# Optimization experiments

Hardware: AMD Instinct MI355X
Metric: run time of the kernel (lower is better)

## Reference

```python
import jax, jax.numpy as jnp
import numpy as np

N, E, D, H, C = 100000, 1600000, 128, 128, 47
EPS = 1e-5


def setup_inputs() -> dict:
    key = jax.random.key(0)
    ks = jax.random.split(key, 10)
    s = 1.0 / np.sqrt(D).astype(np.float32)
    return {
        "x": jax.random.normal(ks[0], (N, D), jnp.float32),
        "edge_index": jax.random.randint(ks[1], (2, E), 0, N, jnp.int32),
        "Wl0": jax.random.normal(ks[2], (H, D), jnp.float32) * s,
        "bl0": jnp.zeros((H,), jnp.float32),
        "Wr0": jax.random.normal(ks[3], (H, D), jnp.float32) * s,
        "g0": jnp.ones((H,), jnp.float32),
        "b0": jnp.zeros((H,), jnp.float32),
        "Wl1": jax.random.normal(ks[4], (H, H), jnp.float32) * s,
        "bl1": jnp.zeros((H,), jnp.float32),
        "Wr1": jax.random.normal(ks[5], (H, H), jnp.float32) * s,
        "g1": jnp.ones((H,), jnp.float32),
        "b1": jnp.zeros((H,), jnp.float32),
        "Wl2": jax.random.normal(ks[6], (C, H), jnp.float32) * s,
        "bl2": jnp.zeros((C,), jnp.float32),
        "Wr2": jax.random.normal(ks[7], (C, H), jnp.float32) * s,
    }


def _sage_conv(x, edge_index, Wl, bl, Wr):
    # PyG SAGEConv(mean aggr): out = lin_l(mean_{j in N(i)} x_j) + lin_r(x_i)
    dst, src = edge_index[0], edge_index[1]
    n = x.shape[0]
    msg = x[src]                                             # [E, d] gather
    summed = jax.ops.segment_sum(msg, dst, num_segments=n)   # [N, d] scatter-add
    deg = jax.ops.segment_sum(jnp.ones((msg.shape[0],), x.dtype), dst, num_segments=n)
    agg = summed / jnp.maximum(deg, 1.0)[:, None]            # mean over neighbors
    return agg @ Wl.T + bl + x @ Wr.T


def _bn(x, g, b):
    # BatchNorm1d, training-mode batch statistics (biased variance)
    mu = jnp.mean(x, axis=0)
    var = jnp.mean(jnp.square(x - mu), axis=0)
    return (x - mu) * jax.lax.rsqrt(var + EPS) * g + b


def reference(x, edge_index, Wl0, bl0, Wr0, g0, b0, Wl1, bl1, Wr1, g1, b1, Wl2, bl2, Wr2):
    h = _sage_conv(x, edge_index, Wl0, bl0, Wr0)
    h = jax.nn.relu(_bn(h, g0, b0))          # dropout treated as identity (deterministic reference)
    h = _sage_conv(h, edge_index, Wl1, bl1, Wr1)
    h = jax.nn.relu(_bn(h, g1, b1))
    return _sage_conv(h, edge_index, Wl2, bl2, Wr2)
```

## Files before the change

kernel.cpp:

```cpp
#include <hip/hip_runtime.h>

typedef __attribute__((ext_vector_type(8))) short short8;
typedef __attribute__((ext_vector_type(4))) float f32x4;

constexpr float BN_EPS = 1e-5f;
#define NBUCKETS 128
#define SLOT 24576

__device__ __forceinline__ ushort f2bf(float f) {
  uint u = __float_as_uint(f);
  u = (u + 0x7fffu + ((u >> 16) & 1u)) >> 16;
  return (ushort)u;
}
__device__ __forceinline__ float bf2f(ushort h) { return __uint_as_float((uint)h << 16); }
__device__ __forceinline__ float bf2f_lo(uint v) { return __uint_as_float(v << 16); }
__device__ __forceinline__ float bf2f_hi(uint v) { return __uint_as_float(v & 0xffff0000u); }

typedef __attribute__((address_space(1))) const unsigned int* as1_cu32;
typedef __attribute__((address_space(3))) unsigned int* as3_u32;
__device__ __forceinline__ void gload_lds16(const void* g, void* l) {
  __builtin_amdgcn_global_load_lds((as1_cu32)g, (as3_u32)l, 16, 0, 0);
}


__global__ __launch_bounds__(256) void k_cast(const float* __restrict__ in, ushort* __restrict__ out, int n4) {
  for (int i = blockIdx.x * 256 + threadIdx.x; i < n4; i += gridDim.x * 256) {
    float4 v = reinterpret_cast<const float4*>(in)[i];
    ushort4 o;
    o.x = f2bf(v.x); o.y = f2bf(v.y); o.z = f2bf(v.z); o.w = f2bf(v.w);
    reinterpret_cast<ushort4*>(out)[i] = o;
  }
}

__global__ __launch_bounds__(256) void k_prep_init(const float* __restrict__ Wl0, const float* __restrict__ Wr0,
                                                   const float* __restrict__ Wl1, const float* __restrict__ Wr1,
                                                   const float* __restrict__ Wl2, const float* __restrict__ Wr2,
                                                   ushort* __restrict__ W0l, ushort* __restrict__ W0r,
                                                   ushort* __restrict__ W1l, ushort* __restrict__ W1r,
                                                   ushort* __restrict__ Wc, int* __restrict__ bcur,
                                                   float* __restrict__ statsAll, int C) {
  int b = blockIdx.x;
  if (b < 64) {
    const float* src = (b < 16) ? Wl0 : (b < 32) ? Wr0 : (b < 48) ? Wl1 : Wr1;
    ushort* dst = (b < 16) ? W0l : (b < 32) ? W0r : (b < 48) ? W1l : W1r;
    int i = (b & 15) * 256 + threadIdx.x;
    float4 v = reinterpret_cast<const float4*>(src)[i];
    ushort4 o;
    o.x = f2bf(v.x); o.y = f2bf(v.y); o.z = f2bf(v.z); o.w = f2bf(v.w);
    reinterpret_cast<ushort4*>(dst)[i] = o;
  } else if (b < 128) {
    int i = (b - 64) * 256 + threadIdx.x;
    int r = i >> 7, k = i & 127;
    float v = 0.f;
    if (r < C) v = Wl2[r * 128 + k];
    else if (r >= 64 && r < 64 + C) v = Wr2[(r - 64) * 128 + k];
    Wc[i] = f2bf(v);
  } else {
    if (threadIdx.x < NBUCKETS) bcur[threadIdx.x] = threadIdx.x * SLOT;
    for (int i = threadIdx.x; i < 512; i += 256) statsAll[i] = 0.f;
  }
}


__global__ __launch_bounds__(256) void k_binscatter(const int* __restrict__ dst, const int* __restrict__ src, int E,
                                                    int* __restrict__ bcur, uint* __restrict__ ebuf) {
  __shared__ int h[NBUCKETS];
  __shared__ int base[NBUCKETS];
  __shared__ int cur[NBUCKETS];
  const int e0 = blockIdx.x * 8192;
  const int e1 = min(e0 + 8192, E);
  for (int i = threadIdx.x; i < NBUCKETS; i += 256) h[i] = 0;
  __syncthreads();
  for (int e = e0 + threadIdx.x * 4; e < e1; e += 1024) {
    int4 d = *reinterpret_cast<const int4*>(&dst[e]);
    if (e + 3 < e1) {
      atomicAdd(&h[d.x >> 10], 1); atomicAdd(&h[d.y >> 10], 1);
      atomicAdd(&h[d.z >> 10], 1); atomicAdd(&h[d.w >> 10], 1);
    } else {
      for (int j = 0; e + j < e1; ++j) atomicAdd(&h[dst[e + j] >> 10], 1);
    }
  }
  __syncthreads();
  if (threadIdx.x < NBUCKETS) {
    base[threadIdx.x] = atomicAdd(&bcur[threadIdx.x], h[threadIdx.x]);
    cur[threadIdx.x] = 0;
  }
  __syncthreads();
  for (int e = e0 + threadIdx.x * 4; e < e1; e += 1024) {
    int4 d = *reinterpret_cast<const int4*>(&dst[e]);
    int4 s = *reinterpret_cast<const int4*>(&src[e]);
    int dd[4] = {d.x, d.y, d.z, d.w};
    int ss[4] = {s.x, s.y, s.z, s.w};
    for (int j = 0; j < 4 && e + j < e1; ++j) {
      int b = dd[j] >> 10;
      int pos = base[b] + atomicAdd(&cur[b], 1);
      ebuf[pos] = (uint)(dd[j] & 1023) | ((uint)ss[j] << 10);
    }
  }
}

__global__ __launch_bounds__(512) void k_bucket_build(const uint* __restrict__ ebuf, const int* __restrict__ bend,
                                                      int* __restrict__ rp, int* __restrict__ deg,
                                                      float* __restrict__ deg_inv, int* __restrict__ csr, int N) {
  __shared__ int cnt[1024];
  __shared__ int pre[1024];
  __shared__ int tmp[1024];
  const int blk = blockIdx.x, tid = threadIdx.x;
  const int base = blk << 10;
  const int p0 = blk * SLOT, p1 = bend[blk];
  for (int i = tid; i < 1024; i += 512) cnt[i] = 0;
  __syncthreads();
  for (int p = p0 + tid; p < p1; p += 512) atomicAdd(&cnt[ebuf[p] & 1023u], 1);
  __syncthreads();
  for (int i = tid; i < 1024; i += 512) pre[i] = cnt[i];
  __syncthreads();
  for (int off = 1; off < 1024; off <<= 1) {
    for (int i = tid; i < 1024; i += 512) tmp[i] = (i >= off) ? pre[i - off] : 0;
    __syncthreads();
    for (int i = tid; i < 1024; i += 512) pre[i] += tmp[i];
    __syncthreads();
  }
  for (int i = tid; i < 1024; i += 512) {
    int node = base + i;
    if (node < N) {
      int c = cnt[i];
      rp[node] = p0 + pre[i] - c;
      deg[node] = c;
      deg_inv[node] = 1.0f / (float)max(c, 1);
    }
    tmp[i] = pre[i] - cnt[i];
  }
  __syncthreads();
  for (int p = p0 + tid; p < p1; p += 512) {
    uint pr = ebuf[p];
    int pos = p0 + atomicAdd(&tmp[pr & 1023u], 1);
    csr[pos] = (int)(pr >> 10);
  }
}


__global__ __launch_bounds__(512, 4) void k_fused(const ushort* __restrict__ X, const ushort* __restrict__ Bsrc,
                                                  const ushort* __restrict__ WA, const ushort* __restrict__ WB,
                                                  const int* __restrict__ rp, const int* __restrict__ deg,
                                                  const float* __restrict__ deg_inv, const int* __restrict__ csr,
                                                  float* __restrict__ partial, ushort* __restrict__ Z, int M) {
  __shared__ ushort sA[64 * 128];
  __shared__ ushort sB[64 * 128];
  const int tid = threadIdx.x;
  const int wave = tid >> 6, lane = tid & 63;
  const int rfrag = lane & 15, kgrp = lane >> 4;
  const int li = rfrag;
  const int row0 = blockIdx.x * 64;

#pragma unroll
  for (int i = 0; i < 2; ++i) {
    int c = wave * 2 + i;
    int lb = c * 1024 + lane * 16;
    int row = lb >> 8, bin = lb & 255;
    int gr = min(row0 + row, M - 1);
    int sb = bin ^ ((row & 7) << 4);
    gload_lds16((const char*)Bsrc + (size_t)gr * 256 + sb, (char*)sB + c * 1024);
  }

  const uint4* X16 = reinterpret_cast<const uint4*>(X);
#pragma unroll
  for (int g = 0; g < 2; ++g) {
    const int lrow = wave * 8 + g * 4 + kgrp;
    const int node = row0 + lrow;
    float a0 = 0.f, a1 = 0.f, a2 = 0.f, a3 = 0.f, a4 = 0.f, a5 = 0.f, a6 = 0.f, a7 = 0.f;
    if (node < M) {
      const int start = rp[node];
      const int c = deg[node];
      int p = 0;
      for (; p + 7 < c; p += 8) {
        int idx[8];
#pragma unroll
        for (int u = 0; u < 8; ++u) idx[u] = csr[start + p + u];
        uint4 v[8];
#pragma unroll
        for (int u = 0; u < 8; ++u) v[u] = X16[(size_t)idx[u] * 16 + li];
#pragma unroll
        for (int u = 0; u < 8; ++u) {
          a0 += bf2f_lo(v[u].x); a1 += bf2f_hi(v[u].x);
          a2 += bf2f_lo(v[u].y); a3 += bf2f_hi(v[u].y);
          a4 += bf2f_lo(v[u].z); a5 += bf2f_hi(v[u].z);
          a6 += bf2f_lo(v[u].w); a7 += bf2f_hi(v[u].w);
        }
      }
      if (p + 3 < c) {
        int idx[4];
#pragma unroll
        for (int u = 0; u < 4; ++u) idx[u] = csr[start + p + u];
        uint4 v[4];
#pragma unroll
        for (int u = 0; u < 4; ++u) v[u] = X16[(size_t)idx[u] * 16 + li];
#pragma unroll
        for (int u = 0; u < 4; ++u) {
          a0 += bf2f_lo(v[u].x); a1 += bf2f_hi(v[u].x);
          a2 += bf2f_lo(v[u].y); a3 += bf2f_hi(v[u].y);
          a4 += bf2f_lo(v[u].z); a5 += bf2f_hi(v[u].z);
          a6 += bf2f_lo(v[u].w); a7 += bf2f_hi(v[u].w);
        }
        p += 4;
      }
      for (; p < c; ++p) {
        uint4 v = X16[(size_t)csr[start + p] * 16 + li];
        a0 += bf2f_lo(v.x); a1 += bf2f_hi(v.x);
        a2 += bf2f_lo(v.y); a3 += bf2f_hi(v.y);
        a4 += bf2f_lo(v.z); a5 += bf2f_hi(v.z);
        a6 += bf2f_lo(v.w); a7 += bf2f_hi(v.w);
      }
      const float di = deg_inv[node];
      a0 *= di; a1 *= di; a2 *= di; a3 *= di;
      a4 *= di; a5 *= di; a6 *= di; a7 *= di;
    }
    uint4 o;
    o.x = (uint)f2bf(a0) | ((uint)f2bf(a1) << 16);
    o.y = (uint)f2bf(a2) | ((uint)f2bf(a3) << 16);
    o.z = (uint)f2bf(a4) | ((uint)f2bf(a5) << 16);
    o.w = (uint)f2bf(a6) | ((uint)f2bf(a7) << 16);
    *reinterpret_cast<uint4*>((char*)sA + lrow * 256 + ((li * 16) ^ ((lrow & 7) << 4))) = o;
  }

  short8 wfA[4], wfB[4];
  {
    const ushort* wa = WA + (wave * 16 + rfrag) * 128 + kgrp * 8;
    const ushort* wb = WB + (wave * 16 + rfrag) * 128 + kgrp * 8;
#pragma unroll
    for (int s = 0; s < 4; ++s) {
      wfA[s] = *reinterpret_cast<const short8*>(wa + s * 32);
      wfB[s] = *reinterpret_cast<const short8*>(wb + s * 32);
    }
  }
  __syncthreads();

  f32x4 acc[4];
#pragma unroll
  for (int i = 0; i < 4; ++i) acc[i] = (f32x4){0.f, 0.f, 0.f, 0.f};

  const int rs = (rfrag & 7) << 4;
#pragma unroll
  for (int strip = 0; strip < 4; ++strip) {
    const int r = strip * 16 + rfrag;
    short8 af[4], bf[4];
#pragma unroll
    for (int s = 0; s < 4; ++s) {
      int off = (kgrp * 16 + s * 64) ^ rs;
      af[s] = *reinterpret_cast<const short8*>((const char*)sA + r * 256 + off);
      bf[s] = *reinterpret_cast<const short8*>((const char*)sB + r * 256 + off);
    }
#pragma unroll
    for (int s = 0; s < 4; ++s)
      acc[strip] = __builtin_amdgcn_mfma_f32_16x16x32_bf16(af[s], wfA[s], acc[strip], 0, 0, 0);
#pragma unroll
    for (int s = 0; s < 4; ++s)
      acc[strip] = __builtin_amdgcn_mfma_f32_16x16x32_bf16(bf[s], wfB[s], acc[strip], 0, 0, 0);
  }

  {
    float s1 = 0.f, s2 = 0.f;
#pragma unroll
    for (int strip = 0; strip < 4; ++strip) {
#pragma unroll
      for (int rr = 0; rr < 4; ++rr) {
        int grow = row0 + strip * 16 + kgrp * 4 + rr;
        if (grow < M) {
          float v = acc[strip][rr];
          s1 += v;
          s2 = fmaf(v, v, s2);
        }
      }
    }
    s1 += __shfl_xor(s1, 16); s2 += __shfl_xor(s2, 16);
    s1 += __shfl_xor(s1, 32); s2 += __shfl_xor(s2, 32);
    if (kgrp == 0) {
      partial[(size_t)blockIdx.x * 256 + wave * 16 + rfrag] = s1;
      partial[(size_t)blockIdx.x * 256 + 128 + wave * 16 + rfrag] = s2;
    }
  }
  __syncthreads();

  const int cb = (wave * 16 + rfrag) * 2;
#pragma unroll
  for (int strip = 0; strip < 4; ++strip) {
#pragma unroll
    for (int rr = 0; rr < 4; ++rr) {
      int row = strip * 16 + kgrp * 4 + rr;
      *reinterpret_cast<ushort*>((char*)sA + row * 256 + (cb ^ ((row & 7) << 4))) = f2bf(acc[strip][rr]);
    }
  }
  __syncthreads();

#pragma unroll
  for (int i = 0; i < 2; ++i) {
    int lb = (wave * 2 + i) * 1024 + lane * 16;
    int row = lb >> 8, bin = lb & 255;
    int gr = row0 + row;
    if (gr < M)
      *reinterpret_cast<uint4*>((char*)Z + (size_t)gr * 256 + bin) =
          *reinterpret_cast<const uint4*>((const char*)sA + row * 256 + (bin ^ ((row & 7) << 4)));
  }
}


__global__ __launch_bounds__(512, 6) void k_gemm1(const ushort* __restrict__ H, const ushort* __restrict__ Wc,
                                                  ushort* __restrict__ Yb, ushort* __restrict__ Rb, int M) {
  __shared__ ushort sA[64 * 128];
  const int tid = threadIdx.x;
  const int wave = tid >> 6, lane = tid & 63;
  const int rfrag = lane & 15, kgrp = lane >> 4;
  const int row0 = blockIdx.x * 64;

#pragma unroll
  for (int i = 0; i < 2; ++i) {
    int c = wave * 2 + i;
    int lb = c * 1024 + lane * 16;
    int row = lb >> 8, bin = lb & 255;
    int gr = min(row0 + row, M - 1);
    int sb = bin ^ ((row & 7) << 4);
    gload_lds16((const char*)H + (size_t)gr * 256 + sb, (char*)sA + c * 1024);
  }

  short8 wf[4];
  {
    const ushort* wp = Wc + (wave * 16 + rfrag) * 128 + kgrp * 8;
#pragma unroll
    for (int s = 0; s < 4; ++s) wf[s] = *reinterpret_cast<const short8*>(wp + s * 32);
  }
  __syncthreads();

  f32x4 acc[4];
#pragma unroll
  for (int i = 0; i < 4; ++i) acc[i] = (f32x4){0.f, 0.f, 0.f, 0.f};
  const int rs = (rfrag & 7) << 4;
#pragma unroll
  for (int strip = 0; strip < 4; ++strip) {
    const int r = strip * 16 + rfrag;
    short8 af[4];
#pragma unroll
    for (int s = 0; s < 4; ++s)
      af[s] = *reinterpret_cast<const short8*>((const char*)sA + r * 256 + ((kgrp * 16 + s * 64) ^ rs));
#pragma unroll
    for (int s = 0; s < 4; ++s)
      acc[strip] = __builtin_amdgcn_mfma_f32_16x16x32_bf16(af[s], wf[s], acc[strip], 0, 0, 0);
  }
  __syncthreads();

  const int cb = (wave * 16 + rfrag) * 2;
#pragma unroll
  for (int strip = 0; strip < 4; ++strip) {
#pragma unroll
    for (int rr = 0; rr < 4; ++rr) {
      int row = strip * 16 + kgrp * 4 + rr;
      *reinterpret_cast<ushort*>((char*)sA + row * 256 + (cb ^ ((row & 7) << 4))) = f2bf(acc[strip][rr]);
    }
  }
  __syncthreads();

#pragma unroll
  for (int i = 0; i < 2; ++i) {
    int lb = (wave * 2 + i) * 1024 + lane * 16;
    int row = lb >> 8, bin = lb & 255;
    int gr = row0 + row;
    if (gr < M) {
      uint4 v = *reinterpret_cast<const uint4*>((const char*)sA + row * 256 + (bin ^ ((row & 7) << 4)));
      if (bin < 128) *reinterpret_cast<uint4*>((char*)Yb + (size_t)gr * 128 + bin) = v;
      else *reinterpret_cast<uint4*>((char*)Rb + (size_t)gr * 128 + (bin - 128)) = v;
    }
  }
}


__global__ __launch_bounds__(256) void k_bn_reduce(const float* __restrict__ partial, int nblk,
                                                   float* __restrict__ stats) {
  float acc = 0.f;
  for (int b = blockIdx.x; b < nblk; b += gridDim.x) acc += partial[(size_t)b * 256 + threadIdx.x];
  atomicAdd(&stats[threadIdx.x], acc);
}

__global__ __launch_bounds__(256) void k_bn_relu(uint2* __restrict__ Z, int n2, const float* __restrict__ sums,
                                                 const float* __restrict__ g, const float* __restrict__ b,
                                                 float invM) {
  __shared__ float ss[256];
  if (threadIdx.x < 128) {
    int f = threadIdx.x;
    float mean = sums[f] * invM;
    float var = fmaxf(sums[128 + f] * invM - mean * mean, 0.f);
    float sc = g[f] * rsqrtf(var + BN_EPS);
    ss[f] = sc;
    ss[128 + f] = fmaf(-mean, sc, b[f]);
  }
  __syncthreads();
  for (int i = blockIdx.x * 256 + threadIdx.x; i < n2; i += gridDim.x * 256) {
    uint2 v = Z[i];
    int f0 = (i & 31) * 4;
    float a0 = fmaxf(fmaf(bf2f_lo(v.x), ss[f0 + 0], ss[128 + f0 + 0]), 0.f);
    float a1 = fmaxf(fmaf(bf2f_hi(v.x), ss[f0 + 1], ss[128 + f0 + 1]), 0.f);
    float a2 = fmaxf(fmaf(bf2f_lo(v.y), ss[f0 + 2], ss[128 + f0 + 2]), 0.f);
    float a3 = fmaxf(fmaf(bf2f_hi(v.y), ss[f0 + 3], ss[128 + f0 + 3]), 0.f);
    v.x = (uint)f2bf(a0) | ((uint)f2bf(a1) << 16);
    v.y = (uint)f2bf(a2) | ((uint)f2bf(a3) << 16);
    Z[i] = v;
  }
}


__global__ __launch_bounds__(256) void k_agg47(const ushort* __restrict__ Yb, const ushort* __restrict__ Rb,
                                               const float* __restrict__ bias, const int* __restrict__ rp,
                                               const int* __restrict__ deg, const float* __restrict__ deg_inv,
                                               const int* __restrict__ csr, float* __restrict__ out,
                                               int N, int C) {
  const int wave = threadIdx.x >> 6, lane = threadIdx.x & 63;
  const int sub = lane >> 3, li = lane & 7;
  const int node = blockIdx.x * 32 + wave * 8 + sub;
  if (node >= N) return;
  const int start = rp[node];
  const int c = deg[node];
  const uint4* Y16 = reinterpret_cast<const uint4*>(Yb);
  float a0 = 0.f, a1 = 0.f, a2 = 0.f, a3 = 0.f, a4 = 0.f, a5 = 0.f, a6 = 0.f, a7 = 0.f;
  int p = 0;
  for (; p + 7 < c; p += 8) {
    int idx[8];
#pragma unroll
    for (int u = 0; u < 8; ++u) idx[u] = csr[start + p + u];
    uint4 v[8];
#pragma unroll
    for (int u = 0; u < 8; ++u) v[u] = Y16[(size_t)idx[u] * 8 + li];
#pragma unroll
    for (int u = 0; u < 8; ++u) {
      a0 += bf2f_lo(v[u].x); a1 += bf2f_hi(v[u].x);
      a2 += bf2f_lo(v[u].y); a3 += bf2f_hi(v[u].y);
      a4 += bf2f_lo(v[u].z); a5 += bf2f_hi(v[u].z);
      a6 += bf2f_lo(v[u].w); a7 += bf2f_hi(v[u].w);
    }
  }
  for (; p < c; ++p) {
    uint4 v = Y16[(size_t)csr[start + p] * 8 + li];
    a0 += bf2f_lo(v.x); a1 += bf2f_hi(v.x);
    a2 += bf2f_lo(v.y); a3 += bf2f_hi(v.y);
    a4 += bf2f_lo(v.z); a5 += bf2f_hi(v.z);
    a6 += bf2f_lo(v.w); a7 += bf2f_hi(v.w);
  }
  const float di = deg_inv[node];
  uint4 sv = reinterpret_cast<const uint4*>(Rb)[(size_t)node * 8 + li];
  float s[8] = {bf2f_lo(sv.x), bf2f_hi(sv.x), bf2f_lo(sv.y), bf2f_hi(sv.y),
                bf2f_lo(sv.z), bf2f_hi(sv.z), bf2f_lo(sv.w), bf2f_hi(sv.w)};
  float a[8] = {a0, a1, a2, a3, a4, a5, a6, a7};
#pragma unroll
  for (int j = 0; j < 8; ++j) {
    int f = li * 8 + j;
    if (f < C) out[(size_t)node * C + f] = fmaf(a[j], di, s[j] + bias[f]);
  }
}


extern "C" void kernel_launch(void* const* d_in, const int* in_sizes, int n_in,
                              void* d_out, int out_size, void* d_ws, size_t ws_size,
                              hipStream_t stream) {
  const float* x   = (const float*)d_in[0];
  const int*   ei  = (const int*)d_in[1];
  const float* Wl0 = (const float*)d_in[2];
  const float* Wr0 = (const float*)d_in[4];
  const float* g0  = (const float*)d_in[5];
  const float* b0  = (const float*)d_in[6];
  const float* Wl1 = (const float*)d_in[7];
  const float* Wr1 = (const float*)d_in[9];
  const float* g1  = (const float*)d_in[10];
  const float* b1  = (const float*)d_in[11];
  const float* Wl2 = (const float*)d_in[12];
  const float* bl2 = (const float*)d_in[13];
  const float* Wr2 = (const float*)d_in[14];

  const int N = in_sizes[0] / 128;
  const int E = in_sizes[1] / 2;
  const int C = in_sizes[13];

  const int* edst = ei;
  const int* esrc = ei + E;

  char* w = (char*)d_ws;
  auto al = [](size_t v) { return (v + 255) & ~(size_t)255; };
  size_t off = 0;
  int*    bcur    = (int*)(w + off);    off = al(off + NBUCKETS * 4);
  float*  stats   = (float*)(w + off);  off = al(off + 512 * 4);
  int*    rp      = (int*)(w + off);    off = al(off + (size_t)N * 4);
  int*    deg     = (int*)(w + off);    off = al(off + (size_t)N * 4);
  float*  deg_inv = (float*)(w + off);  off = al(off + (size_t)N * 4);
  int*    csr     = (int*)(w + off);    off = al(off + (size_t)NBUCKETS * SLOT * 4);
  uint*   ebuf    = (uint*)(w + off);   off = al(off + (size_t)NBUCKETS * SLOT * 4);
  ushort* Xb      = (ushort*)(w + off); off = al(off + (size_t)N * 128 * 2);
  ushort* hA      = (ushort*)(w + off); off = al(off + (size_t)N * 128 * 2);
  ushort* hB      = (ushort*)(w + off); off = al(off + (size_t)N * 128 * 2);
  ushort* W0l     = (ushort*)(w + off); off = al(off + 16384 * 2);
  ushort* W0r     = (ushort*)(w + off); off = al(off + 16384 * 2);
  ushort* W1l     = (ushort*)(w + off); off = al(off + 16384 * 2);
  ushort* W1r     = (ushort*)(w + off); off = al(off + 16384 * 2);
  ushort* Wc      = (ushort*)(w + off); off = al(off + 16384 * 2);
  const int nblkG = (N + 63) / 64;
  float*  partial = (float*)(w + off);  off = al(off + (size_t)nblkG * 256 * 4);

  float* stats0 = stats;
  float* stats1 = stats + 256;
  ushort* Yb = hB;
  ushort* Rb = hB + (size_t)N * 64;

  const int binGrid = (E + 8191) / 8192;
  const int nbBuck = (N + 1023) / 1024;
  const int agg47Grid = (N + 31) / 32;
  const float invM = 1.0f / (float)N;

  k_cast<<<2048, 256, 0, stream>>>(x, Xb, N * 32);
  k_prep_init<<<129, 256, 0, stream>>>(Wl0, Wr0, Wl1, Wr1, Wl2, Wr2, W0l, W0r, W1l, W1r, Wc,
                                       bcur, stats, C);

  k_binscatter<<<binGrid, 256, 0, stream>>>(edst, esrc, E, bcur, ebuf);
  k_bucket_build<<<nbBuck, 512, 0, stream>>>(ebuf, bcur, rp, deg, deg_inv, csr, N);

  k_fused<<<nblkG, 512, 0, stream>>>(Xb, Xb, W0l, W0r, rp, deg, deg_inv, csr, partial, hB, N);
  k_bn_reduce<<<64, 256, 0, stream>>>(partial, nblkG, stats0);
  k_bn_relu<<<2048, 256, 0, stream>>>((uint2*)hB, N * 32, stats0, g0, b0, invM);

  k_fused<<<nblkG, 512, 0, stream>>>(hB, hB, W1l, W1r, rp, deg, deg_inv, csr, partial, hA, N);
  k_bn_reduce<<<64, 256, 0, stream>>>(partial, nblkG, stats1);
  k_bn_relu<<<2048, 256, 0, stream>>>((uint2*)hA, N * 32, stats1, g1, b1, invM);

  k_gemm1<<<nblkG, 512, 0, stream>>>(hA, Wc, Yb, Rb, N);
  k_agg47<<<agg47Grid, 256, 0, stream>>>(Yb, Rb, bl2, rp, deg, deg_inv, csr, (float*)d_out, N, C);
}
```

Measured before the change: 314.1 us.

## Fuse BN+ReLU into consumer kernels and merge prep kernels into one launch

Removes the separate BN-reduce and BN-ReLU passes. Per-block statistics are now accumulated with global atomics, and the normalize+ReLU step is applied on the fly by the next kernel: inside the neighbor gather, on the self-row tile in LDS, and in the final GEMM. The cast, weight-prep and edge bin-scatter kernels are merged into one launch, with bucket cursors reset by a memset. In exchange, every gathered neighbor row now pays extra FMAs, and float atomics make the statistics order-dependent.

```diff
diff --git a/kernel.cpp b/kernel.cpp
--- a/kernel.cpp
+++ b/kernel.cpp
@@ -23,80 +23,85 @@
 }
 
 
-__global__ __launch_bounds__(256) void k_cast(const float* __restrict__ in, ushort* __restrict__ out, int n4) {
-  for (int i = blockIdx.x * 256 + threadIdx.x; i < n4; i += gridDim.x * 256) {
-    float4 v = reinterpret_cast<const float4*>(in)[i];
+__global__ __launch_bounds__(256) void k_prep(const int* __restrict__ dst, const int* __restrict__ src, int E,
+                                              int* __restrict__ bcur, uint* __restrict__ ebuf,
+                                              const float* __restrict__ x, ushort* __restrict__ Xb, int n4,
+                                              const float* __restrict__ Wl0, const float* __restrict__ Wr0,
+                                              const float* __restrict__ Wl1, const float* __restrict__ Wr1,
+                                              const float* __restrict__ Wl2, const float* __restrict__ Wr2,
+                                              ushort* __restrict__ W0l, ushort* __restrict__ W0r,
+                                              ushort* __restrict__ W1l, ushort* __restrict__ W1r,
+                                              ushort* __restrict__ Wc, float* __restrict__ statsAll,
+                                              int C, int binGrid, int castGrid) {
+  int bb = blockIdx.x;
+  if (bb < binGrid) {
+    __shared__ int h[NBUCKETS];
+    __shared__ int base[NBUCKETS];
+    __shared__ int cur[NBUCKETS];
+    const int e0 = bb * 8192;
+    const int e1 = min(e0 + 8192, E);
+    for (int i = threadIdx.x; i < NBUCKETS; i += 256) h[i] = 0;
+    __syncthreads();
+    for (int e = e0 + threadIdx.x * 4; e < e1; e += 1024) {
+      int4 d = *reinterpret_cast<const int4*>(&dst[e]);
+      if (e + 3 < e1) {
+        atomicAdd(&h[d.x >> 10], 1); atomicAdd(&h[d.y >> 10], 1);
+        atomicAdd(&h[d.z >> 10], 1); atomicAdd(&h[d.w >> 10], 1);
+      } else {
+        for (int j = 0; e + j < e1; ++j) atomicAdd(&h[dst[e + j] >> 10], 1);
+      }
+    }
+    __syncthreads();
+    if (threadIdx.x < NBUCKETS) {
+      base[threadIdx.x] = threadIdx.x * SLOT + atomicAdd(&bcur[threadIdx.x], h[threadIdx.x]);
+      cur[threadIdx.x] = 0;
+    }
+    __syncthreads();
+    for (int e = e0 + threadIdx.x * 4; e < e1; e += 1024) {
+      int4 d = *reinterpret_cast<const int4*>(&dst[e]);
+      int4 s = *reinterpret_cast<const int4*>(&src[e]);
+      int dd[4] = {d.x, d.y, d.z, d.w};
+      int ss[4] = {s.x, s.y, s.z, s.w};
+      for (int j = 0; j < 4 && e + j < e1; ++j) {
+        int b = dd[j] >> 10;
+        int pos = base[b] + atomicAdd(&cur[b], 1);
+        ebuf[pos] = (uint)(dd[j] & 1023) | ((uint)ss[j] << 10);
+      }
+    }
+    return;
+  }
+  bb -= binGrid;
+  if (bb < 64) {
+    const float* s = (bb < 16) ? Wl0 : (bb < 32) ? Wr0 : (bb < 48) ? Wl1 : Wr1;
+    ushort* d = (bb < 16) ? W0l : (bb < 32) ? W0r : (bb < 48) ? W1l : W1r;
+    int i = (bb & 15) * 256 + threadIdx.x;
+    float4 v = reinterpret_cast<const float4*>(s)[i];
     ushort4 o;
     o.x = f2bf(v.x); o.y = f2bf(v.y); o.z = f2bf(v.z); o.w = f2bf(v.w);
-    reinterpret_cast<ushort4*>(out)[i] = o;
-  }
-}
-
-__global__ __launch_bounds__(256) void k_prep_init(const float* __restrict__ Wl0, const float* __restrict__ Wr0,
-                                                   const float* __restrict__ Wl1, const float* __restrict__ Wr1,
-                                                   const float* __restrict__ Wl2, const float* __restrict__ Wr2,
-                                                   ushort* __restrict__ W0l, ushort* __restrict__ W0r,
-                                                   ushort* __restrict__ W1l, ushort* __restrict__ W1r,
-                                                   ushort* __restrict__ Wc, int* __restrict__ bcur,
-                                                   float* __restrict__ statsAll, int C) {
-  int b = blockIdx.x;
-  if (b < 64) {
-    const float* src = (b < 16) ? Wl0 : (b < 32) ? Wr0 : (b < 48) ? Wl1 : Wr1;
-    ushort* dst = (b < 16) ? W0l : (b < 32) ? W0r : (b < 48) ? W1l : W1r;
-    int i = (b & 15) * 256 + threadIdx.x;
-    float4 v = reinterpret_cast<const float4*>(src)[i];
-    ushort4 o;
-    o.x = f2bf(v.x); o.y = f2bf(v.y); o.z = f2bf(v.z); o.w = f2bf(v.w);
-    reinterpret_cast<ushort4*>(dst)[i] = o;
-  } else if (b < 128) {
-    int i = (b - 64) * 256 + threadIdx.x;
+    reinterpret_cast<ushort4*>(d)[i] = o;
+    return;
+  }
+  bb -= 64;
+  if (bb < 64) {
+    int i = bb * 256 + threadIdx.x;
     int r = i >> 7, k = i & 127;
     float v = 0.f;
     if (r < C) v = Wl2[r * 128 + k];
     else if (r >= 64 && r < 64 + C) v = Wr2[(r - 64) * 128 + k];
     Wc[i] = f2bf(v);
-  } else {
-    if (threadIdx.x < NBUCKETS) bcur[threadIdx.x] = threadIdx.x * SLOT;
-    for (int i = threadIdx.x; i < 512; i += 256) statsAll[i] = 0.f;
-  }
-}
-
-
-__global__ __launch_bounds__(256) void k_binscatter(const int* __restrict__ dst, const int* __restrict__ src, int E,
-                                                    int* __restrict__ bcur, uint* __restrict__ ebuf) {
-  __shared__ int h[NBUCKETS];
-  __shared__ int base[NBUCKETS];
-  __shared__ int cur[NBUCKETS];
-  const int e0 = blockIdx.x * 8192;
-  const int e1 = min(e0 + 8192, E);
-  for (int i = threadIdx.x; i < NBUCKETS; i += 256) h[i] = 0;
-  __syncthreads();
-  for (int e = e0 + threadIdx.x * 4; e < e1; e += 1024) {
-    int4 d = *reinterpret_cast<const int4*>(&dst[e]);
-    if (e + 3 < e1) {
-      atomicAdd(&h[d.x >> 10], 1); atomicAdd(&h[d.y >> 10], 1);
-      atomicAdd(&h[d.z >> 10], 1); atomicAdd(&h[d.w >> 10], 1);
-    } else {
-      for (int j = 0; e + j < e1; ++j) atomicAdd(&h[dst[e + j] >> 10], 1);
-    }
-  }
-  __syncthreads();
-  if (threadIdx.x < NBUCKETS) {
-    base[threadIdx.x] = atomicAdd(&bcur[threadIdx.x], h[threadIdx.x]);
-    cur[threadIdx.x] = 0;
-  }
-  __syncthreads();
-  for (int e = e0 + threadIdx.x * 4; e < e1; e += 1024) {
-    int4 d = *reinterpret_cast<const int4*>(&dst[e]);
-    int4 s = *reinterpret_cast<const int4*>(&src[e]);
-    int dd[4] = {d.x, d.y, d.z, d.w};
-    int ss[4] = {s.x, s.y, s.z, s.w};
-    for (int j = 0; j < 4 && e + j < e1; ++j) {
-      int b = dd[j] >> 10;
-      int pos = base[b] + atomicAdd(&cur[b], 1);
-      ebuf[pos] = (uint)(dd[j] & 1023) | ((uint)ss[j] << 10);
-    }
-  }
+    return;
+  }
+  bb -= 64;
+  if (bb < castGrid) {
+    for (int i = bb * 256 + threadIdx.x; i < n4; i += castGrid * 256) {
+      float4 v = reinterpret_cast<const float4*>(x)[i];
+      ushort4 o;
+      o.x = f2bf(v.x); o.y = f2bf(v.y); o.z = f2bf(v.z); o.w = f2bf(v.w);
+      reinterpret_cast<ushort4*>(Xb)[i] = o;
+    }
+    return;
+  }
+  for (int i = threadIdx.x; i < 512; i += 256) statsAll[i] = 0.f;
 }
 
 __global__ __launch_bounds__(512) void k_bucket_build(const uint* __restrict__ ebuf, const int* __restrict__ bend,
@@ -107,7 +112,7 @@
   __shared__ int tmp[1024];
   const int blk = blockIdx.x, tid = threadIdx.x;
   const int base = blk << 10;
-  const int p0 = blk * SLOT, p1 = bend[blk];
+  const int p0 = blk * SLOT, p1 = p0 + bend[blk];
   for (int i = tid; i < 1024; i += 512) cnt[i] = 0;
   __syncthreads();
   for (int p = p0 + tid; p < p1; p += 512) atomicAdd(&cnt[ebuf[p] & 1023u], 1);
@@ -139,18 +144,31 @@
 }
 
 
+template <bool PRE_BN>
 __global__ __launch_bounds__(512, 4) void k_fused(const ushort* __restrict__ X, const ushort* __restrict__ Bsrc,
                                                   const ushort* __restrict__ WA, const ushort* __restrict__ WB,
                                                   const int* __restrict__ rp, const int* __restrict__ deg,
                                                   const float* __restrict__ deg_inv, const int* __restrict__ csr,
-                                                  float* __restrict__ partial, ushort* __restrict__ Z, int M) {
+                                                  const float* __restrict__ sums, const float* __restrict__ gw,
+                                                  const float* __restrict__ bw, float invM,
+                                                  float* __restrict__ stats_out, ushort* __restrict__ Z, int M) {
   __shared__ ushort sA[64 * 128];
   __shared__ ushort sB[64 * 128];
+  __shared__ float ssc[PRE_BN ? 128 : 1];
+  __shared__ float ssh[PRE_BN ? 128 : 1];
   const int tid = threadIdx.x;
   const int wave = tid >> 6, lane = tid & 63;
   const int rfrag = lane & 15, kgrp = lane >> 4;
   const int li = rfrag;
   const int row0 = blockIdx.x * 64;
+
+  if (PRE_BN && tid < 128) {
+    float mean = sums[tid] * invM;
+    float var = fmaxf(sums[128 + tid] * invM - mean * mean, 0.f);
+    float sc = gw[tid] * rsqrtf(var + BN_EPS);
+    ssc[tid] = sc;
+    ssh[tid] = fmaf(-mean, sc, bw[tid]);
+  }
 
 #pragma unroll
   for (int i = 0; i < 2; ++i) {
@@ -160,6 +178,28 @@
     int gr = min(row0 + row, M - 1);
     int sb = bin ^ ((row & 7) << 4);
     gload_lds16((const char*)Bsrc + (size_t)gr * 256 + sb, (char*)sB + c * 1024);
+  }
+
+  float scr[8], shr[8];
+  if (PRE_BN) {
+#pragma unroll
+    for (int e = 0; e < 8; ++e) {
+      int f = li * 8 + e;
+      float mean = sums[f] * invM;
+      float var = fmaxf(sums[128 + f] * invM - mean * mean, 0.f);
+      scr[e] = gw[f] * rsqrtf(var + BN_EPS);
+      shr[e] = fmaf(-mean, scr[e], bw[f]);
+    }
+  }
+
+#define BN8(vv, A0, A1, e0)                                                     \
+  {                                                                             \
+    float xl = bf2f_lo(vv), xh = bf2f_hi(vv);                                   \
+    if (PRE_BN) {                                                               \
+      xl = fmaxf(fmaf(xl, scr[e0], shr[e0]), 0.f);                              \
+      xh = fmaxf(fmaf(xh, scr[e0 + 1], shr[e0 + 1]), 0.f);                      \
+    }                                                                           \
+    A0 += xl; A1 += xh;                                                         \
   }
 
   const uint4* X16 = reinterpret_cast<const uint4*>(X);
@@ -181,10 +221,8 @@
         for (int u = 0; u < 8; ++u) v[u] = X16[(size_t)idx[u] * 16 + li];
 #pragma unroll
         for (int u = 0; u < 8; ++u) {
-          a0 += bf2f_lo(v[u].x); a1 += bf2f_hi(v[u].x);
-          a2 += bf2f_lo(v[u].y); a3 += bf2f_hi(v[u].y);
-          a4 += bf2f_lo(v[u].z); a5 += bf2f_hi(v[u].z);
-          a6 += bf2f_lo(v[u].w); a7 += bf2f_hi(v[u].w);
+          BN8(v[u].x, a0, a1, 0); BN8(v[u].y, a2, a3, 2);
+          BN8(v[u].z, a4, a5, 4); BN8(v[u].w, a6, a7, 6);
         }
       }
       if (p + 3 < c) {
@@ -196,19 +234,15 @@
         for (int u = 0; u < 4; ++u) v[u] = X16[(size_t)idx[u] * 16 + li];
 #pragma unroll
         for (int u = 0; u < 4; ++u) {
-          a0 += bf2f_lo(v[u].x); a1 += bf2f_hi(v[u].x);
-          a2 += bf2f_lo(v[u].y); a3 += bf2f_hi(v[u].y);
-          a4 += bf2f_lo(v[u].z); a5 += bf2f_hi(v[u].z);
-          a6 += bf2f_lo(v[u].w); a7 += bf2f_hi(v[u].w);
+          BN8(v[u].x, a0, a1, 0); BN8(v[u].y, a2, a3, 2);
+          BN8(v[u].z, a4, a5, 4); BN8(v[u].w, a6, a7, 6);
         }
         p += 4;
       }
       for (; p < c; ++p) {
         uint4 v = X16[(size_t)csr[start + p] * 16 + li];
-        a0 += bf2f_lo(v.x); a1 += bf2f_hi(v.x);
-        a2 += bf2f_lo(v.y); a3 += bf2f_hi(v.y);
-        a4 += bf2f_lo(v.z); a5 += bf2f_hi(v.z);
-        a6 += bf2f_lo(v.w); a7 += bf2f_hi(v.w);
+        BN8(v.x, a0, a1, 0); BN8(v.y, a2, a3, 2);
+        BN8(v.z, a4, a5, 4); BN8(v.w, a6, a7, 6);
       }
       const float di = deg_inv[node];
       a0 *= di; a1 *= di; a2 *= di; a3 *= di;
@@ -221,6 +255,7 @@
     o.w = (uint)f2bf(a6) | ((uint)f2bf(a7) << 16);
     *reinterpret_cast<uint4*>((char*)sA + lrow * 256 + ((li * 16) ^ ((lrow & 7) << 4))) = o;
   }
+#undef BN8
 
   short8 wfA[4], wfB[4];
   {
@@ -233,6 +268,27 @@
     }
   }
   __syncthreads();
+
+  if (PRE_BN) {
+#pragma unroll
+    for (int i = 0; i < 2; ++i) {
+      int addr = (wave * 2 + i) * 1024 + lane * 16;
+      int row = addr >> 8, bin = addr & 255;
+      int col0 = (bin ^ ((row & 7) << 4)) >> 1;
+      uint4 v = *reinterpret_cast<const uint4*>((const char*)sB + addr);
+      uint vv[4] = {v.x, v.y, v.z, v.w};
+      uint ov[4];
+#pragma unroll
+      for (int q = 0; q < 4; ++q) {
+        int f = col0 + q * 2;
+        float xl = fmaxf(fmaf(bf2f_lo(vv[q]), ssc[f], ssh[f]), 0.f);
+        float xh = fmaxf(fmaf(bf2f_hi(vv[q]), ssc[f + 1], ssh[f + 1]), 0.f);
+        ov[q] = (uint)f2bf(xl) | ((uint)f2bf(xh) << 16);
+      }
+      *reinterpret_cast<uint4*>((char*)sB + addr) = make_uint4(ov[0], ov[1], ov[2], ov[3]);
+    }
+    __syncthreads();
+  }
 
   f32x4 acc[4];
 #pragma unroll
@@ -274,8 +330,8 @@
     s1 += __shfl_xor(s1, 16); s2 += __shfl_xor(s2, 16);
     s1 += __shfl_xor(s1, 32); s2 += __shfl_xor(s2, 32);
     if (kgrp == 0) {
-      partial[(size_t)blockIdx.x * 256 + wave * 16 + rfrag] = s1;
-      partial[(size_t)blockIdx.x * 256 + 128 + wave * 16 + rfrag] = s2;
+      atomicAdd(&stats_out[wave * 16 + rfrag], s1);
+      atomicAdd(&stats_out[128 + wave * 16 + rfrag], s2);
     }
   }
   __syncthreads();
@@ -304,12 +360,24 @@
 
 
 __global__ __launch_bounds__(512, 6) void k_gemm1(const ushort* __restrict__ H, const ushort* __restrict__ Wc,
+                                                  const float* __restrict__ sums, const float* __restrict__ gw,
+                                                  const float* __restrict__ bw, float invM,
                                                   ushort* __restrict__ Yb, ushort* __restrict__ Rb, int M) {
   __shared__ ushort sA[64 * 128];
+  __shared__ float ssc[128];
+  __shared__ float ssh[128];
   const int tid = threadIdx.x;
   const int wave = tid >> 6, lane = tid & 63;
   const int rfrag = lane & 15, kgrp = lane >> 4;
   const int row0 = blockIdx.x * 64;
+
+  if (tid < 128) {
+    float mean = sums[tid] * invM;
+    float var = fmaxf(sums[128 + tid] * invM - mean * mean, 0.f);
+    float sc = gw[tid] * rsqrtf(var + BN_EPS);
+    ssc[tid] = sc;
+    ssh[tid] = fmaf(-mean, sc, bw[tid]);
+  }
 
 #pragma unroll
   for (int i = 0; i < 2; ++i) {
@@ -326,6 +394,25 @@
     const ushort* wp = Wc + (wave * 16 + rfrag) * 128 + kgrp * 8;
 #pragma unroll
     for (int s = 0; s < 4; ++s) wf[s] = *reinterpret_cast<const short8*>(wp + s * 32);
+  }
+  __syncthreads();
+
+#pragma unroll
+  for (int i = 0; i < 2; ++i) {
+    int addr = (wave * 2 + i) * 1024 + lane * 16;
+    int row = addr >> 8, bin = addr & 255;
+    int col0 = (bin ^ ((row & 7) << 4)) >> 1;
+    uint4 v = *reinterpret_cast<const uint4*>((const char*)sA + addr);
+    uint vv[4] = {v.x, v.y, v.z, v.w};
+    uint ov[4];
+#pragma unroll
+    for (int q = 0; q < 4; ++q) {
+      int f = col0 + q * 2;
+      float xl = fmaxf(fmaf(bf2f_lo(vv[q]), ssc[f], ssh[f]), 0.f);
+      float xh = fmaxf(fmaf(bf2f_hi(vv[q]), ssc[f + 1], ssh[f + 1]), 0.f);
+      ov[q] = (uint)f2bf(xl) | ((uint)f2bf(xh) << 16);
+    }
+    *reinterpret_cast<uint4*>((char*)sA + addr) = make_uint4(ov[0], ov[1], ov[2], ov[3]);
   }
   __syncthreads();
 
@@ -367,40 +454,6 @@
       if (bin < 128) *reinterpret_cast<uint4*>((char*)Yb + (size_t)gr * 128 + bin) = v;
       else *reinterpret_cast<uint4*>((char*)Rb + (size_t)gr * 128 + (bin - 128)) = v;
     }
-  }
-}
-
-
-__global__ __launch_bounds__(256) void k_bn_reduce(const float* __restrict__ partial, int nblk,
-                                                   float* __restrict__ stats) {
-  float acc = 0.f;
-  for (int b = blockIdx.x; b < nblk; b += gridDim.x) acc += partial[(size_t)b * 256 + threadIdx.x];
-  atomicAdd(&stats[threadIdx.x], acc);
-}
-
-__global__ __launch_bounds__(256) void k_bn_relu(uint2* __restrict__ Z, int n2, const float* __restrict__ sums,
-                                                 const float* __restrict__ g, const float* __restrict__ b,
-                                                 float invM) {
-  __shared__ float ss[256];
-  if (threadIdx.x < 128) {
-    int f = threadIdx.x;
-    float mean = sums[f] * invM;
-    float var = fmaxf(sums[128 + f] * invM - mean * mean, 0.f);
-    float sc = g[f] * rsqrtf(var + BN_EPS);
-    ss[f] = sc;
-    ss[128 + f] = fmaf(-mean, sc, b[f]);
-  }
-  __syncthreads();
-  for (int i = blockIdx.x * 256 + threadIdx.x; i < n2; i += gridDim.x * 256) {
-    uint2 v = Z[i];
-    int f0 = (i & 31) * 4;
-    float a0 = fmaxf(fmaf(bf2f_lo(v.x), ss[f0 + 0], ss[128 + f0 + 0]), 0.f);
-    float a1 = fmaxf(fmaf(bf2f_hi(v.x), ss[f0 + 1], ss[128 + f0 + 1]), 0.f);
-    float a2 = fmaxf(fmaf(bf2f_lo(v.y), ss[f0 + 2], ss[128 + f0 + 2]), 0.f);
-    float a3 = fmaxf(fmaf(bf2f_hi(v.y), ss[f0 + 3], ss[128 + f0 + 3]), 0.f);
-    v.x = (uint)f2bf(a0) | ((uint)f2bf(a1) << 16);
-    v.y = (uint)f2bf(a2) | ((uint)f2bf(a3) << 16);
-    Z[i] = v;
   }
 }
 
@@ -496,8 +549,6 @@
   ushort* W1l     = (ushort*)(w + off); off = al(off + 16384 * 2);
   ushort* W1r     = (ushort*)(w + off); off = al(off + 16384 * 2);
   ushort* Wc      = (ushort*)(w + off); off = al(off + 16384 * 2);
-  const int nblkG = (N + 63) / 64;
-  float*  partial = (float*)(w + off);  off = al(off + (size_t)nblkG * 256 * 4);
 
   float* stats0 = stats;
   float* stats1 = stats + 256;
@@ -505,25 +556,26 @@
   ushort* Rb = hB + (size_t)N * 64;
 
   const int binGrid = (E + 8191) / 8192;
+  const int castGrid = 384;
   const int nbBuck = (N + 1023) / 1024;
+  const int nblkG = (N + 63) / 64;
   const int agg47Grid = (N + 31) / 32;
   const float invM = 1.0f / (float)N;
 
-  k_cast<<<2048, 256, 0, stream>>>(x, Xb, N * 32);
-  k_prep_init<<<129, 256, 0, stream>>>(Wl0, Wr0, Wl1, Wr1, Wl2, Wr2, W0l, W0r, W1l, W1r, Wc,
-                                       bcur, stats, C);
-
-  k_binscatter<<<binGrid, 256, 0, stream>>>(edst, esrc, E, bcur, ebuf);
+  hipMemsetAsync(bcur, 0, NBUCKETS * 4, stream);
+
+  k_prep<<<binGrid + 128 + castGrid + 1, 256, 0, stream>>>(
+      edst, esrc, E, bcur, ebuf, x, Xb, N * 32,
+      Wl0, Wr0, Wl1, Wr1, Wl2, Wr2, W0l, W0r, W1l, W1r, Wc, stats, C, binGrid, castGrid);
+
   k_bucket_build<<<nbBuck, 512, 0, stream>>>(ebuf, bcur, rp, deg, deg_inv, csr, N);
 
-  k_fused<<<nblkG, 512, 0, stream>>>(Xb, Xb, W0l, W0r, rp, deg, deg_inv, csr, partial, hB, N);
-  k_bn_reduce<<<64, 256, 0, stream>>>(partial, nblkG, stats0);
-  k_bn_relu<<<2048, 256, 0, stream>>>((uint2*)hB, N * 32, stats0, g0, b0, invM);
-
-  k_fused<<<nblkG, 512, 0, stream>>>(hB, hB, W1l, W1r, rp, deg, deg_inv, csr, partial, hA, N);
-  k_bn_reduce<<<64, 256, 0, stream>>>(partial, nblkG, stats1);
-  k_bn_relu<<<2048, 256, 0, stream>>>((uint2*)hA, N * 32, stats1, g1, b1, invM);
-
-  k_gemm1<<<nblkG, 512, 0, stream>>>(hA, Wc, Yb, Rb, N);
+  k_fused<false><<<nblkG, 512, 0, stream>>>(Xb, Xb, W0l, W0r, rp, deg, deg_inv, csr,
+                                            nullptr, nullptr, nullptr, 0.f, stats0, hB, N);
+
+  k_fused<true><<<nblkG, 512, 0, stream>>>(hB, hB, W1l, W1r, rp, deg, deg_inv, csr,
+                                           stats0, g0, b0, invM, stats1, hA, N);
+
+  k_gemm1<<<nblkG, 512, 0, stream>>>(hA, Wc, stats1, g1, b1, invM, Yb, Rb, N);
   k_agg47<<<agg47Grid, 256, 0, stream>>>(Yb, Rb, bl2, rp, deg, deg_inv, csr, (float*)d_out, N, C);
 }
```

Result: slower. 353.0 us (+12.4%).
